# Performance work log

Hardware: AMD Instinct MI355X
Metric: run time of the kernel (lower is better)

The kernel has to match this reference:

```python
import jax, jax.numpy as jnp
import numpy as np

B, S, H = 8, 2048, 1024
G, K = 16, 320          # n_groups, codebook_size
D = H // G              # codebook_dim per group


def setup_inputs() -> dict:
    key = jax.random.key(0)
    k1, k2, k3, k4 = jax.random.split(key, 4)
    inputs = jax.random.normal(k1, (B, S, H), jnp.float32)
    attention_mask = jax.random.uniform(k2, (B, S)) < 0.9
    W_cb = jax.random.normal(k3, (D, K), jnp.float32) * 0.05  # shared codebook projection
    b_cb = jnp.zeros((K,), jnp.float32)
    codevectors = jax.random.normal(k4, (K, D), jnp.float32) * 0.05
    return {"inputs": inputs, "attention_mask": attention_mask,
            "W_cb": W_cb, "b_cb": b_cb, "codevectors": codevectors}


def reference(inputs, attention_mask, W_cb, b_cb, codevectors):
    # inputs: [B,S,H]; split H into G groups of D (tensor_split, dim=-1)
    Bs, Ss, Hs = inputs.shape
    Ks, Ds = codevectors.shape
    Gs = Hs // Ds
    x = inputs.reshape(Bs, Ss, Gs, Ds)                              # [B,S,G,D]
    logits = jnp.einsum('bsgd,dk->bsgk', x, W_cb) + b_cb            # grouped codebook logits
    # training path, gumbel_softmax=False: probs = log_softmax(logits).exp() = softmax
    probs = jax.nn.softmax(logits, axis=-1)                         # [B,S,G,K]
    cv = jnp.einsum('bsgk,kd->bsgd', probs, codevectors)            # choice(probs, codevectors)
    cv = cv.reshape(Bs, Ss, Hs)
    # scatter back into zero-padded tensors: positions outside the mask stay zero
    cv = jnp.where(attention_mask[:, :, None], cv, 0.0)             # [B,S,H]
    codewords = jnp.argmax(logits, axis=-1)                         # [B,S,G]
    codewords = jnp.where(attention_mask[:, :, None], codewords, 0)
    return cv, codewords
```

## Files before the change

kernel.cpp:

```cpp
#include <hip/hip_runtime.h>
#include <math.h>

typedef _Float16 f16;
typedef _Float16 f16x2 __attribute__((ext_vector_type(2)));
typedef _Float16 f16x4 __attribute__((ext_vector_type(4)));
typedef _Float16 f16x8 __attribute__((ext_vector_type(8)));
typedef short short8 __attribute__((ext_vector_type(8)));
typedef float f32x4 __attribute__((ext_vector_type(4)));

#define NROWS (8 * 2048 * 16)
#define BLOCK 512
#define WAVES 8
#define NITER 8
#define GRID 256
#define TAU2 4.4e-4f
#define LOG2E 1.4426950408889634f
#define MEXP 6.0f
#define EXP2F(x) __builtin_amdgcn_exp2f(x)

__device__ __forceinline__ short f2bf(float f) {
    unsigned u = __builtin_bit_cast(unsigned, f);
    return (short)((u + 0x7fffu + ((u >> 16) & 1u)) >> 16);
}
__device__ __forceinline__ float bf2f(short h) {
    return __builtin_bit_cast(float, ((unsigned)(unsigned short)h) << 16);
}
__device__ __forceinline__ f16x2 pkrtz(float a, float b) {
    return __builtin_bit_cast(f16x2, __builtin_amdgcn_cvt_pkrtz(a, b));
}

template <int HB>
__device__ __forceinline__ void half_pass(
    const short* __restrict__ Wh, const short* __restrict__ Wl,
    const f16* __restrict__ CVf2, const float* __restrict__ bs,
    const short8 (&xh)[2], const short8 (&xl)[2],
    int l15, int lg, int wb0, int wb1, int bsb, int cvlo, int cvhi,
    f32x4 (&cv)[4], float& sum_run,
    float& m1o, float& m2o, int& i1o, int& c0, int& c1, int& c2)
{
    f32x4 acc[10];
    #pragma unroll
    for (int nt = 0; nt < 10; ++nt) {
        const int ntg = HB / 16 + nt;
        acc[nt] = *(const f32x4*)&bs[ntg * 16 + bsb];
        short8 whf0 = *(const short8*)&Wh[ntg * 1024 + wb0];
        short8 wlf0 = *(const short8*)&Wl[ntg * 1024 + wb0];
        acc[nt] = __builtin_amdgcn_mfma_f32_16x16x32_bf16(whf0, xl[0], acc[nt], 0, 0, 0);
        acc[nt] = __builtin_amdgcn_mfma_f32_16x16x32_bf16(wlf0, xh[0], acc[nt], 0, 0, 0);
        acc[nt] = __builtin_amdgcn_mfma_f32_16x16x32_bf16(whf0, xh[0], acc[nt], 0, 0, 0);
        short8 whf1 = *(const short8*)&Wh[ntg * 1024 + wb1];
        short8 wlf1 = *(const short8*)&Wl[ntg * 1024 + wb1];
        acc[nt] = __builtin_amdgcn_mfma_f32_16x16x32_bf16(whf1, xl[1], acc[nt], 0, 0, 0);
        acc[nt] = __builtin_amdgcn_mfma_f32_16x16x32_bf16(wlf1, xh[1], acc[nt], 0, 0, 0);
        acc[nt] = __builtin_amdgcn_mfma_f32_16x16x32_bf16(whf1, xh[1], acc[nt], 0, 0, 0);
    }

    float m1a = -INFINITY, m2a = -INFINITY, m1b = -INFINITY, m2b = -INFINITY;
    int i1a = HB, i1b = HB + 80;
    #pragma unroll
    for (int nt = 0; nt < 5; ++nt) {
        #pragma unroll
        for (int r = 0; r < 4; ++r) {
            float va = acc[nt][r];
            m2a = fmaxf(m2a, fminf(m1a, va));
            if (va > m1a) { m1a = va; i1a = HB + nt * 16 + lg * 4 + r; }
            float vb = acc[nt + 5][r];
            m2b = fmaxf(m2b, fminf(m1b, vb));
            if (vb > m1b) { m1b = vb; i1b = HB + (nt + 5) * 16 + lg * 4 + r; }
        }
    }

    float sA = 0.f, sB = 0.f, sC = 0.f, sD = 0.f;
    #pragma unroll
    for (int nt = 0; nt < 10; ++nt) {
        const int ntg = HB / 16 + nt;
        float p0 = EXP2F(acc[nt][0] - MEXP);
        float p1 = EXP2F(acc[nt][1] - MEXP);
        float p2 = EXP2F(acc[nt][2] - MEXP);
        float p3 = EXP2F(acc[nt][3] - MEXP);
        sA += p0; sB += p1; sC += p2; sD += p3;
        f16x2 plo = pkrtz(p0, p1);
        f16x2 phi = pkrtz(p2, p3);
        f16x4 pf = {plo[0], plo[1], phi[0], phi[1]};
        f16x8 lo = *(const f16x8*)&CVf2[ntg * 1024 + cvlo];
        f16x8 hi = *(const f16x8*)&CVf2[ntg * 1024 + cvhi];
        f16x4 cf0 = __builtin_shufflevector(lo, lo, 0, 1, 2, 3);
        f16x4 cf1 = __builtin_shufflevector(lo, lo, 4, 5, 6, 7);
        f16x4 cf2 = __builtin_shufflevector(hi, hi, 0, 1, 2, 3);
        f16x4 cf3 = __builtin_shufflevector(hi, hi, 4, 5, 6, 7);
        cv[0] = __builtin_amdgcn_mfma_f32_16x16x16f16(cf0, pf, cv[0], 0, 0, 0);
        cv[1] = __builtin_amdgcn_mfma_f32_16x16x16f16(cf1, pf, cv[1], 0, 0, 0);
        cv[2] = __builtin_amdgcn_mfma_f32_16x16x16f16(cf2, pf, cv[2], 0, 0, 0);
        cv[3] = __builtin_amdgcn_mfma_f32_16x16x16f16(cf3, pf, cv[3], 0, 0, 0);
    }
    sum_run += (sA + sB) + (sC + sD);

    float m2 = fmaxf(fmaxf(m2a, m2b), fminf(m1a, m1b));
    float m1 = m1a;
    int i1 = i1a;
    if (m1b > m1) { m1 = m1b; i1 = i1b; }
    #pragma unroll
    for (int dx = 16; dx <= 32; dx <<= 1) {
        float mo = __shfl_xor(m1, dx, 64);
        int io = __shfl_xor(i1, dx, 64);
        float m2x = __shfl_xor(m2, dx, 64);
        m2 = fmaxf(fmaxf(m2, m2x), fminf(m1, mo));
        if (mo > m1 || (mo == m1 && io < i1)) { m1 = mo; i1 = io; }
    }

    c0 = -1; c1 = -1; c2 = -1;
    if (m1 - m2 < TAU2) {
        const float thr = m1 - TAU2;
        #pragma unroll
        for (int nt = 0; nt < 10; ++nt) {
            #pragma unroll
            for (int r = 0; r < 4; ++r) {
                if (acc[nt][r] >= thr) {
                    int c = HB + nt * 16 + lg * 4 + r;
                    if (c0 < 0) c0 = c;
                    else if (c1 < 0) c1 = c;
                    else if (c2 < 0) c2 = c;
                }
            }
        }
    }
    m1o = m1; m2o = m2; i1o = i1;
}

__global__ __launch_bounds__(BLOCK) void vq_mfma(
    const float* __restrict__ inputs,
    const int* __restrict__ mask,
    const float* __restrict__ Wcb,
    const float* __restrict__ bcb,
    const float* __restrict__ codevec,
    float* __restrict__ out_cv,
    float* __restrict__ out_cw)
{
    __shared__ __align__(16) short Wh[320 * 64];
    __shared__ __align__(16) short Wl[320 * 64];
    __shared__ __align__(16) f16 CVf2[20 * 1024];
    __shared__ __align__(16) float bs[320];

    const int tid = threadIdx.x;

    for (int e = tid; e < 64 * 320; e += BLOCK) {
        int d = e / 320, n = e - d * 320;
        float w = Wcb[e] * LOG2E;
        short wh = f2bf(w);
        short wl = f2bf(w - bf2f(wh));
        int s = d >> 3;
        int idx = n * 64 + (((s ^ n) & 7) << 3) + (d & 7);
        Wh[idx] = wh;
        Wl[idx] = wl;
    }
    for (int e = tid; e < 320 * 64; e += BLOCK) {
        int c = e >> 6, d = e & 63;
        int lgs = (c >> 2) & 3, s = (d >> 5) & 1;
        int slot = (lgs * 2 + s) ^ (d & 7);
        CVf2[(c >> 4) * 1024 + (d & 15) * 64 + slot * 8 + ((d >> 4) & 1) * 4 + (c & 3)] =
            (f16)codevec[e];
    }
    for (int e = tid; e < 320; e += BLOCK) bs[e] = bcb[e] * LOG2E;
    __syncthreads();

    const int wid = tid >> 6;
    const int lane = tid & 63;
    const int l15 = lane & 15;
    const int lg = lane >> 4;
    const int l7 = l15 & 7;
    const int u = blockIdx.x * WAVES + wid;

    const int wb0 = l15 * 64 + (((lg ^ l7) & 7) << 3);
    const int wb1 = l15 * 64 + ((((4 + lg) ^ l7) & 7) << 3);
    const int bsb = lg * 4;
    const int cvlo = l15 * 64 + (((lg * 2) ^ l7) << 3);
    const int cvhi = l15 * 64 + (((lg * 2 + 1) ^ l7) << 3);

    #pragma unroll 1
    for (int it = 0; it < NITER; ++it) {
        const int row0 = u * (NITER * 16) + it * 16;
        const float* xrow = inputs + (size_t)(row0 + l15) * 64;

        short8 xh[2], xl[2];
        #pragma unroll
        for (int kc = 0; kc < 2; ++kc) {
            float4 a = *(const float4*)(xrow + kc * 32 + lg * 8);
            float4 b = *(const float4*)(xrow + kc * 32 + lg * 8 + 4);
            float xv[8] = {a.x, a.y, a.z, a.w, b.x, b.y, b.z, b.w};
            short8 h, l;
            #pragma unroll
            for (int e = 0; e < 8; ++e) {
                short hh = f2bf(xv[e]);
                h[e] = hh;
                l[e] = f2bf(xv[e] - bf2f(hh));
            }
            xh[kc] = h;
            xl[kc] = l;
        }

        f32x4 cv[4];
        #pragma unroll
        for (int dt = 0; dt < 4; ++dt) cv[dt] = (f32x4){0.f, 0.f, 0.f, 0.f};
        float sum_run = 0.f;
        float m1A, m2A, m1B, m2B;
        int i1A, i1B, cA0, cA1, cA2, cB0, cB1, cB2;

        half_pass<0>(Wh, Wl, CVf2, bs, xh, xl, l15, lg,
                     wb0, wb1, bsb, cvlo, cvhi,
                     cv, sum_run, m1A, m2A, i1A, cA0, cA1, cA2);
        half_pass<160>(Wh, Wl, CVf2, bs, xh, xl, l15, lg,
                       wb0, wb1, bsb, cvlo, cvhi,
                       cv, sum_run, m1B, m2B, i1B, cB0, cB1, cB2);

        float m1 = m1A;
        int i1 = i1A;
        float m2 = fmaxf(fmaxf(m2A, m2B), fminf(m1A, m1B));
        if (m1B > m1) { m1 = m1B; i1 = i1B; }

        float sum = sum_run;
        sum += __shfl_xor(sum, 16, 64);
        sum += __shfl_xor(sum, 32, 64);

        const int mk = mask[u * NITER + it];
        int cw = i1;
        const bool flag = mk && (m1 - m2 < TAU2);
        if (__any(flag)) {
            float bv = -INFINITY;
            int bi = 0x7fffffff;
            #pragma unroll 1
            for (int t = 0; t < 8; ++t) {
                int c = (t == 0) ? i1A : (t == 1) ? i1B :
                        (t == 2) ? cA0 : (t == 3) ? cA1 : (t == 4) ? cA2 :
                        (t == 5) ? cB0 : (t == 6) ? cB1 : cB2;
                if (!flag) c = -1;
                if (__any(c >= 0)) {
                    if (c >= 0) {
                        float sacc = bcb[c];
                        #pragma unroll 4
                        for (int q = 0; q < 16; ++q) {
                            float4 xv4 = *(const float4*)(xrow + q * 4);
                            sacc = fmaf(xv4.x, Wcb[(q * 4 + 0) * 320 + c], sacc);
                            sacc = fmaf(xv4.y, Wcb[(q * 4 + 1) * 320 + c], sacc);
                            sacc = fmaf(xv4.z, Wcb[(q * 4 + 2) * 320 + c], sacc);
                            sacc = fmaf(xv4.w, Wcb[(q * 4 + 3) * 320 + c], sacc);
                        }
                        if (sacc > bv || (sacc == bv && c < bi)) { bv = sacc; bi = c; }
                    }
                }
            }
            #pragma unroll
            for (int dx = 16; dx <= 32; dx <<= 1) {
                float vo = __shfl_xor(bv, dx, 64);
                int io = __shfl_xor(bi, dx, 64);
                if (vo > bv || (vo == bv && io < bi)) { bv = vo; bi = io; }
            }
            if (flag) cw = bi;
        }

        const float inv = mk ? (1.0f / sum) : 0.0f;
        float* orow = out_cv + (size_t)(row0 + l15) * 64;
        #pragma unroll
        for (int dt = 0; dt < 4; ++dt) {
            f32x4 v;
            v[0] = cv[dt][0] * inv;
            v[1] = cv[dt][1] * inv;
            v[2] = cv[dt][2] * inv;
            v[3] = cv[dt][3] * inv;
            *(f32x4*)(orow + dt * 16 + lg * 4) = v;
        }
        if (lg == 0) out_cw[row0 + l15] = mk ? (float)cw : 0.0f;
    }
}

extern "C" void kernel_launch(void* const* d_in, const int* in_sizes, int n_in,
                              void* d_out, int out_size, void* d_ws, size_t ws_size,
                              hipStream_t stream) {
    const float* inputs  = (const float*)d_in[0];
    const int*   mask    = (const int*)d_in[1];
    const float* Wcb     = (const float*)d_in[2];
    const float* bcb     = (const float*)d_in[3];
    const float* codevec = (const float*)d_in[4];

    float* out_cv = (float*)d_out;
    float* out_cw = out_cv + (size_t)NROWS * 64;

    vq_mfma<<<GRID, BLOCK, 0, stream>>>(inputs, mask, Wcb, bcb, codevec,
                                        out_cv, out_cw);
}
```

Measured before the change: 87.52 us.

## Use 16x16x32 f16 MFMA for codevector product and raise MFMA priority

New measurement: 84.03 us. -4.0%, faster.

```diff
diff --git a/kernel.cpp b/kernel.cpp
--- a/kernel.cpp
+++ b/kernel.cpp
@@ -3,7 +3,6 @@
 
 typedef _Float16 f16;
 typedef _Float16 f16x2 __attribute__((ext_vector_type(2)));
-typedef _Float16 f16x4 __attribute__((ext_vector_type(4)));
 typedef _Float16 f16x8 __attribute__((ext_vector_type(8)));
 typedef short short8 __attribute__((ext_vector_type(8)));
 typedef float f32x4 __attribute__((ext_vector_type(4)));
@@ -32,13 +31,14 @@
 template <int HB>
 __device__ __forceinline__ void half_pass(
     const short* __restrict__ Wh, const short* __restrict__ Wl,
-    const f16* __restrict__ CVf2, const float* __restrict__ bs,
+    const f16* __restrict__ CVp, const float* __restrict__ bs,
     const short8 (&xh)[2], const short8 (&xl)[2],
-    int l15, int lg, int wb0, int wb1, int bsb, int cvlo, int cvhi,
+    int l15, int lg, int wb0, int wb1, int bsb, int cvb,
     f32x4 (&cv)[4], float& sum_run,
     float& m1o, float& m2o, int& i1o, int& c0, int& c1, int& c2)
 {
     f32x4 acc[10];
+    __builtin_amdgcn_s_setprio(1);
     #pragma unroll
     for (int nt = 0; nt < 10; ++nt) {
         const int ntg = HB / 16 + nt;
@@ -54,6 +54,7 @@
         acc[nt] = __builtin_amdgcn_mfma_f32_16x16x32_bf16(wlf1, xh[1], acc[nt], 0, 0, 0);
         acc[nt] = __builtin_amdgcn_mfma_f32_16x16x32_bf16(whf1, xh[1], acc[nt], 0, 0, 0);
     }
+    __builtin_amdgcn_s_setprio(0);
 
     float m1a = -INFINITY, m2a = -INFINITY, m1b = -INFINITY, m2b = -INFINITY;
     int i1a = HB, i1b = HB + 80;
@@ -72,26 +73,26 @@
 
     float sA = 0.f, sB = 0.f, sC = 0.f, sD = 0.f;
     #pragma unroll
-    for (int nt = 0; nt < 10; ++nt) {
-        const int ntg = HB / 16 + nt;
-        float p0 = EXP2F(acc[nt][0] - MEXP);
-        float p1 = EXP2F(acc[nt][1] - MEXP);
-        float p2 = EXP2F(acc[nt][2] - MEXP);
-        float p3 = EXP2F(acc[nt][3] - MEXP);
-        sA += p0; sB += p1; sC += p2; sD += p3;
-        f16x2 plo = pkrtz(p0, p1);
-        f16x2 phi = pkrtz(p2, p3);
-        f16x4 pf = {plo[0], plo[1], phi[0], phi[1]};
-        f16x8 lo = *(const f16x8*)&CVf2[ntg * 1024 + cvlo];
-        f16x8 hi = *(const f16x8*)&CVf2[ntg * 1024 + cvhi];
-        f16x4 cf0 = __builtin_shufflevector(lo, lo, 0, 1, 2, 3);
-        f16x4 cf1 = __builtin_shufflevector(lo, lo, 4, 5, 6, 7);
-        f16x4 cf2 = __builtin_shufflevector(hi, hi, 0, 1, 2, 3);
-        f16x4 cf3 = __builtin_shufflevector(hi, hi, 4, 5, 6, 7);
-        cv[0] = __builtin_amdgcn_mfma_f32_16x16x16f16(cf0, pf, cv[0], 0, 0, 0);
-        cv[1] = __builtin_amdgcn_mfma_f32_16x16x16f16(cf1, pf, cv[1], 0, 0, 0);
-        cv[2] = __builtin_amdgcn_mfma_f32_16x16x16f16(cf2, pf, cv[2], 0, 0, 0);
-        cv[3] = __builtin_amdgcn_mfma_f32_16x16x16f16(cf3, pf, cv[3], 0, 0, 0);
+    for (int lp = 0; lp < 5; ++lp) {
+        const int pg = HB / 32 + lp;
+        float q0 = EXP2F(acc[lp * 2][0] - MEXP);
+        float q1 = EXP2F(acc[lp * 2][1] - MEXP);
+        float q2 = EXP2F(acc[lp * 2][2] - MEXP);
+        float q3 = EXP2F(acc[lp * 2][3] - MEXP);
+        float q4 = EXP2F(acc[lp * 2 + 1][0] - MEXP);
+        float q5 = EXP2F(acc[lp * 2 + 1][1] - MEXP);
+        float q6 = EXP2F(acc[lp * 2 + 1][2] - MEXP);
+        float q7 = EXP2F(acc[lp * 2 + 1][3] - MEXP);
+        sA += q0 + q4; sB += q1 + q5; sC += q2 + q6; sD += q3 + q7;
+        f16x2 a01 = pkrtz(q0, q1), a23 = pkrtz(q2, q3);
+        f16x2 a45 = pkrtz(q4, q5), a67 = pkrtz(q6, q7);
+        f16x8 pf = {a01[0], a01[1], a23[0], a23[1],
+                    a45[0], a45[1], a67[0], a67[1]};
+        #pragma unroll
+        for (int dt = 0; dt < 4; ++dt) {
+            f16x8 cf = *(const f16x8*)&CVp[(pg * 4 + dt) * 512 + cvb];
+            cv[dt] = __builtin_amdgcn_mfma_f32_16x16x32_f16(cf, pf, cv[dt], 0, 0, 0);
+        }
     }
     sum_run += (sA + sB) + (sC + sD);
 
@@ -138,7 +139,7 @@
 {
     __shared__ __align__(16) short Wh[320 * 64];
     __shared__ __align__(16) short Wl[320 * 64];
-    __shared__ __align__(16) f16 CVf2[20 * 1024];
+    __shared__ __align__(16) f16 CVp[20480];
     __shared__ __align__(16) float bs[320];
 
     const int tid = threadIdx.x;
@@ -155,9 +156,11 @@
     }
     for (int e = tid; e < 320 * 64; e += BLOCK) {
         int c = e >> 6, d = e & 63;
-        int lgs = (c >> 2) & 3, s = (d >> 5) & 1;
-        int slot = (lgs * 2 + s) ^ (d & 7);
-        CVf2[(c >> 4) * 1024 + (d & 15) * 64 + slot * 8 + ((d >> 4) & 1) * 4 + (c & 3)] =
+        int p = c >> 5, tp = (c >> 4) & 1, tc = c & 15;
+        int lgc = tc >> 2, r = tc & 3;
+        int ee = (tp << 2) | r;
+        int dt = d >> 4, m = d & 15;
+        CVp[(p * 4 + dt) * 512 + m * 32 + (((lgc ^ (m >> 1)) & 3) << 3) + ee] =
             (f16)codevec[e];
     }
     for (int e = tid; e < 320; e += BLOCK) bs[e] = bcb[e] * LOG2E;
@@ -173,8 +176,7 @@
     const int wb0 = l15 * 64 + (((lg ^ l7) & 7) << 3);
     const int wb1 = l15 * 64 + ((((4 + lg) ^ l7) & 7) << 3);
     const int bsb = lg * 4;
-    const int cvlo = l15 * 64 + (((lg * 2) ^ l7) << 3);
-    const int cvhi = l15 * 64 + (((lg * 2 + 1) ^ l7) << 3);
+    const int cvb = l15 * 32 + (((lg ^ (l15 >> 1)) & 3) << 3);
 
     #pragma unroll 1
     for (int it = 0; it < NITER; ++it) {
@@ -205,11 +207,11 @@
         float m1A, m2A, m1B, m2B;
         int i1A, i1B, cA0, cA1, cA2, cB0, cB1, cB2;
 
-        half_pass<0>(Wh, Wl, CVf2, bs, xh, xl, l15, lg,
-                     wb0, wb1, bsb, cvlo, cvhi,
+        half_pass<0>(Wh, Wl, CVp, bs, xh, xl, l15, lg,
+                     wb0, wb1, bsb, cvb,
                      cv, sum_run, m1A, m2A, i1A, cA0, cA1, cA2);
-        half_pass<160>(Wh, Wl, CVf2, bs, xh, xl, l15, lg,
-                       wb0, wb1, bsb, cvlo, cvhi,
+        half_pass<160>(Wh, Wl, CVp, bs, xh, xl, l15, lg,
+                       wb0, wb1, bsb, cvb,
                        cv, sum_run, m1B, m2B, i1B, cB0, cB1, cB2);
 
         float m1 = m1A;
```
